# Kernel optimization log

Hardware: AMD Instinct MI355X
Metric: run time of the kernel (lower is better)

The kernel has to match this reference:

```python
import jax, jax.numpy as jnp
import numpy as np

V, E, H = 32000, 1024, 1024   # vocab, embed, hidden
B, T = 16, 128                 # batch, decode steps
SOS = 1


def setup_inputs() -> dict:
    key = jax.random.key(0)
    ks = jax.random.split(key, 10)
    w = 1.0 / np.sqrt(H)
    return {
        "encoder_outputs": jax.random.normal(ks[0], (B, T, H), jnp.float32),
        "encoder_hidden_h": jax.random.normal(ks[1], (1, B, H), jnp.float32),
        "encoder_hidden_c": jax.random.normal(ks[2], (1, B, H), jnp.float32),
        "embedding": jax.random.normal(ks[3], (V, E), jnp.float32) * 0.02,
        "W_ih": jax.random.normal(ks[4], (4 * H, E), jnp.float32) * w,
        "W_hh": jax.random.normal(ks[5], (4 * H, H), jnp.float32) * w,
        "b_ih": jax.random.normal(ks[6], (4 * H,), jnp.float32) * w,
        "b_hh": jax.random.normal(ks[7], (4 * H,), jnp.float32) * w,
        "W_lin": jax.random.normal(ks[8], (V, H), jnp.float32) * w,
        "b_lin": jax.random.normal(ks[9], (V,), jnp.float32) * w,
    }


def reference(encoder_outputs, encoder_hidden_h, encoder_hidden_c,
              embedding, W_ih, W_hh, b_ih, b_hh, W_lin, b_lin):
    # embed(token) -> single-step LSTM -> linear -> argmax feeds next step.
    batch = encoder_outputs.shape[0]
    num_steps = encoder_outputs.shape[1]
    h0 = encoder_hidden_h[0]  # [B,H] (num_layers=1)
    c0 = encoder_hidden_c[0]
    tok0 = jnp.full((batch,), SOS, dtype=jnp.int32)

    def step(carry, _):
        tok, h, c = carry
        x = embedding[tok]                                   # [B,E] gather
        gates = x @ W_ih.T + b_ih + h @ W_hh.T + b_hh        # [B,4H]
        i, f, g, o = jnp.split(gates, 4, axis=-1)            # PyTorch gate order i,f,g,o
        c = jax.nn.sigmoid(f) * c + jax.nn.sigmoid(i) * jnp.tanh(g)
        h = jax.nn.sigmoid(o) * jnp.tanh(c)
        logits = h @ W_lin.T + b_lin                         # [B,V]
        tok = jnp.argmax(logits, axis=-1).astype(jnp.int32)  # detached greedy token
        return (tok, h, c), logits

    (tok, h, c), logits = jax.lax.scan(step, (tok0, h0, c0), None, length=num_steps)
    # logits: [T,B,V] -> [B,T,V], then log_softmax as in torch forward
    log_probs = jax.nn.log_softmax(jnp.transpose(logits, (1, 0, 2)), axis=-1)
    return log_probs, h[None], c[None]
```

## Files before the change

kernel.cpp:

```cpp
#include <hip/hip_runtime.h>
#include <climits>
#include <cmath>


#define NBLK 256
#define NTHR 512
#define WPB  8
#define Bb 16
#define Hh 1024
#define Vv 32000
#define Tt 128
#define PITCH 1028

typedef float v4f __attribute__((ext_vector_type(4)));

__device__ __forceinline__ float dot4f(v4f a, v4f b, float acc) {
  return fmaf(a.x, b.x, fmaf(a.y, b.y, fmaf(a.z, b.z, fmaf(a.w, b.w, acc))));
}

__device__ __forceinline__ void online_upd(float& m, float& s, int& idx, float v, int r) {
  if (v > m) { s = s * __expf(m - v) + 1.0f; m = v; idx = r; }
  else       { s += __expf(v - m); }
}

__device__ __forceinline__ void merge_ms(float& m, float& s, int& idx,
                                         float m2, float s2, int i2) {
  if (m2 > m)       { s = s * __expf(m - m2) + s2; m = m2; idx = i2; }
  else if (m2 == m) { s += s2; idx = (i2 < idx) ? i2 : idx; }
  else              { s = fmaf(s2, __expf(m2 - m), s); }
}

__device__ __forceinline__ void grid_barrier(int* flags, int* gen, int epoch) {
  __syncthreads();
  if (threadIdx.x == 0) {
    __hip_atomic_store(&flags[blockIdx.x * 16], epoch,
                       __ATOMIC_RELEASE, __HIP_MEMORY_SCOPE_AGENT);
  }
  if (blockIdx.x == 0) {
    if (threadIdx.x < 64) {
      int base = threadIdx.x * 4;
      for (;;) {
        bool done = true;
#pragma unroll
        for (int k = 0; k < 4; ++k) {
          int v = __hip_atomic_load(&flags[(base + k) * 16],
                                    __ATOMIC_RELAXED, __HIP_MEMORY_SCOPE_AGENT);
          done &= (v >= epoch);
        }
        if (done) break;
        __builtin_amdgcn_s_sleep(2);
      }
    }
    __syncthreads();
    if (threadIdx.x == 0) {
      __threadfence();
      __hip_atomic_store(gen, epoch, __ATOMIC_RELEASE, __HIP_MEMORY_SCOPE_AGENT);
    }
  } else {
    if (threadIdx.x == 0) {
      while (__hip_atomic_load(gen, __ATOMIC_RELAXED, __HIP_MEMORY_SCOPE_AGENT) < epoch) {
        __builtin_amdgcn_s_sleep(2);
      }
      __threadfence();
    }
  }
  __syncthreads();
}

extern "C" __global__ void __launch_bounds__(NTHR, 2)
decoder_rnn_kernel(const float* __restrict__ enc_h,
                   const float* __restrict__ enc_c,
                   const float* __restrict__ emb,
                   const float* __restrict__ Wih,
                   const float* __restrict__ Whh,
                   const float* __restrict__ bih,
                   const float* __restrict__ bhh,
                   const float* __restrict__ Wlin,
                   const float* __restrict__ blin,
                   float* __restrict__ out,
                   int* flags, int* gen,
                   float* hb0, float* hb1, float* cbuf,
                   float* pm, float* ps, int* pidx)
{
  __shared__ float x_sh[Bb * PITCH];
  __shared__ float h_sh[Bb * PITCH];
  __shared__ float gpart[WPB][8][Bb];
  __shared__ float bm_[WPB][Bb];
  __shared__ float bs_[WPB][Bb];
  __shared__ int   bi_[WPB][Bb];
  __shared__ int   tk_sh[Bb];
  __shared__ float nm_sh[Bb];

  const int tid  = threadIdx.x;
  const int lane = tid & 63;
  const int wid  = tid >> 6;
  const int q    = lane >> 4;
  const int b    = lane & 15;
  const int bid  = blockIdx.x;
  const int wgl  = bid * WPB + wid;
  int ep = 0;

  float accL[4][4];
#pragma unroll
  for (int g = 0; g < 4; ++g)
#pragma unroll
    for (int r = 0; r < 4; ++r) accL[g][r] = 0.f;

  for (int i = tid; i < Bb * (Hh / 4); i += NTHR) {
    int bb = i >> 8, k4 = i & 255;
    v4f hv = reinterpret_cast<const v4f*>(enc_h + (size_t)bb * Hh)[k4];
    *reinterpret_cast<v4f*>(&h_sh[bb * PITCH + k4 * 4]) = hv;
  }

  for (int t = 0; t < Tt; ++t) {
    float* hcur = (t & 1) ? hb1 : hb0;

    if (t > 0) {
      int g = tid >> 5, l = tid & 31;
      float m = -__builtin_inff(); float s = 0.f; int ix = INT_MAX;
      for (int wb = l; wb < NBLK; wb += 32)
        merge_ms(m, s, ix, pm[wb * Bb + g], ps[wb * Bb + g], pidx[wb * Bb + g]);
#pragma unroll
      for (int off = 16; off; off >>= 1) {
        float m2 = __shfl_xor(m, off, 32);
        float s2 = __shfl_xor(s, off, 32);
        int   i2 = __shfl_xor(ix, off, 32);
        merge_ms(m, s, ix, m2, s2, i2);
      }
      if (l == 0) { tk_sh[g] = ix; nm_sh[g] = m + logf(s); }
    } else {
      if (tid < Bb) tk_sh[tid] = 1;
    }
    __syncthreads();

    if (t > 0 && wgl < 2000 && q == 0) {
      float nb = nm_sh[b];
      size_t obase = ((size_t)b * Tt + (t - 1)) * (size_t)Vv;
#pragma unroll
      for (int g = 0; g < 4; ++g) {
        int rbase = wgl * 16 + g * 4;
        v4f vo;
        vo.x = accL[g][0] - nb; vo.y = accL[g][1] - nb;
        vo.z = accL[g][2] - nb; vo.w = accL[g][3] - nb;
        __builtin_nontemporal_store(vo, reinterpret_cast<v4f*>(out + obase + rbase));
      }
    }
    for (int i = tid; i < Bb * (Hh / 4); i += NTHR) {
      int bb = i >> 8, k4 = i & 255;
      int tk = tk_sh[bb];
      v4f xv = reinterpret_cast<const v4f*>(emb + (size_t)tk * Hh)[k4];
      *reinterpret_cast<v4f*>(&x_sh[bb * PITCH + k4 * 4]) = xv;
    }
    __syncthreads();

    {
      const int j  = bid * 4 + (wid >> 1);
      const int kh = wid & 1;
      const int kb4 = kh * 128 + q * 32;
      const v4f* wi0 = reinterpret_cast<const v4f*>(Wih) + (size_t)j * 256 + kb4;
      const v4f* wi1 = wi0 + (size_t)Hh * 256;
      const v4f* wi2 = wi1 + (size_t)Hh * 256;
      const v4f* wi3 = wi2 + (size_t)Hh * 256;
      const v4f* wh0 = reinterpret_cast<const v4f*>(Whh) + (size_t)j * 256 + kb4;
      const v4f* wh1 = wh0 + (size_t)Hh * 256;
      const v4f* wh2 = wh1 + (size_t)Hh * 256;
      const v4f* wh3 = wh2 + (size_t)Hh * 256;
      const float* xb  = &x_sh[b * PITCH + kh * 512 + q * 128];
      const float* hbp = &h_sh[b * PITCH + kh * 512 + q * 128];
      float a0=0,a1=0,a2=0,a3=0,a4=0,a5=0,a6=0,a7=0;
#pragma unroll 2
      for (int i = 0; i < 32; ++i) {
        v4f xv = *reinterpret_cast<const v4f*>(xb + i * 4);
        v4f hv = *reinterpret_cast<const v4f*>(hbp + i * 4);
        a0 = dot4f(xv, wi0[i], a0);
        a1 = dot4f(xv, wi1[i], a1);
        a2 = dot4f(xv, wi2[i], a2);
        a3 = dot4f(xv, wi3[i], a3);
        a4 = dot4f(hv, wh0[i], a4);
        a5 = dot4f(hv, wh1[i], a5);
        a6 = dot4f(hv, wh2[i], a6);
        a7 = dot4f(hv, wh3[i], a7);
      }
      a0 += __shfl_xor(a0, 16, 64); a0 += __shfl_xor(a0, 32, 64);
      a1 += __shfl_xor(a1, 16, 64); a1 += __shfl_xor(a1, 32, 64);
      a2 += __shfl_xor(a2, 16, 64); a2 += __shfl_xor(a2, 32, 64);
      a3 += __shfl_xor(a3, 16, 64); a3 += __shfl_xor(a3, 32, 64);
      a4 += __shfl_xor(a4, 16, 64); a4 += __shfl_xor(a4, 32, 64);
      a5 += __shfl_xor(a5, 16, 64); a5 += __shfl_xor(a5, 32, 64);
      a6 += __shfl_xor(a6, 16, 64); a6 += __shfl_xor(a6, 32, 64);
      a7 += __shfl_xor(a7, 16, 64); a7 += __shfl_xor(a7, 32, 64);
      if (q == 0) {
        gpart[wid][0][b] = a0; gpart[wid][1][b] = a1;
        gpart[wid][2][b] = a2; gpart[wid][3][b] = a3;
        gpart[wid][4][b] = a4; gpart[wid][5][b] = a5;
        gpart[wid][6][b] = a6; gpart[wid][7][b] = a7;
      }
    }
    __syncthreads();
    if (wid == 0) {
      const int jj = q;
      const int j  = bid * 4 + jj;
      float s0 = gpart[2*jj][0][b] + gpart[2*jj+1][0][b];
      float s1 = gpart[2*jj][1][b] + gpart[2*jj+1][1][b];
      float s2 = gpart[2*jj][2][b] + gpart[2*jj+1][2][b];
      float s3 = gpart[2*jj][3][b] + gpart[2*jj+1][3][b];
      float s4 = gpart[2*jj][4][b] + gpart[2*jj+1][4][b];
      float s5 = gpart[2*jj][5][b] + gpart[2*jj+1][5][b];
      float s6 = gpart[2*jj][6][b] + gpart[2*jj+1][6][b];
      float s7 = gpart[2*jj][7][b] + gpart[2*jj+1][7][b];
      float gi = s0 + s4 + bih[j]          + bhh[j];
      float gf = s1 + s5 + bih[Hh + j]     + bhh[Hh + j];
      float gg = s2 + s6 + bih[2*Hh + j]   + bhh[2*Hh + j];
      float go = s3 + s7 + bih[3*Hh + j]   + bhh[3*Hh + j];
      float cold = (t == 0) ? enc_c[b * Hh + j] : cbuf[b * Hh + j];
      float ig = 1.f / (1.f + expf(-gi));
      float fg = 1.f / (1.f + expf(-gf));
      float og = 1.f / (1.f + expf(-go));
      float cn = fg * cold + ig * tanhf(gg);
      float hn = og * tanhf(cn);
      cbuf[b * Hh + j] = cn;
      hcur[b * Hh + j] = hn;
    }
    grid_barrier(flags, gen, ++ep);

    for (int i = tid; i < Bb * (Hh / 4); i += NTHR) {
      int bb = i >> 8, k4 = i & 255;
      v4f hv = reinterpret_cast<const v4f*>(hcur + (size_t)bb * Hh)[k4];
      *reinterpret_cast<v4f*>(&h_sh[bb * PITCH + k4 * 4]) = hv;
    }
    __syncthreads();
    float mloc = -__builtin_inff(); float sloc = 0.f; int iloc = INT_MAX;
    if (wgl < 2000) {
      const float* hbp = &h_sh[b * PITCH + q * 256];
#pragma unroll
      for (int g = 0; g < 4; ++g) {
        size_t rbase = (size_t)wgl * 16 + g * 4;
        const v4f* w0 = reinterpret_cast<const v4f*>(Wlin) + rbase * 256 + q * 64;
        const v4f* w1 = w0 + 256;
        const v4f* w2 = w1 + 256;
        const v4f* w3 = w2 + 256;
        float a0=0, a1=0, a2=0, a3=0;
#pragma unroll 4
        for (int i = 0; i < 64; ++i) {
          v4f hv = *reinterpret_cast<const v4f*>(hbp + i * 4);
          a0 = dot4f(hv, w0[i], a0);
          a1 = dot4f(hv, w1[i], a1);
          a2 = dot4f(hv, w2[i], a2);
          a3 = dot4f(hv, w3[i], a3);
        }
        a0 += __shfl_xor(a0, 16, 64); a0 += __shfl_xor(a0, 32, 64);
        a1 += __shfl_xor(a1, 16, 64); a1 += __shfl_xor(a1, 32, 64);
        a2 += __shfl_xor(a2, 16, 64); a2 += __shfl_xor(a2, 32, 64);
        a3 += __shfl_xor(a3, 16, 64); a3 += __shfl_xor(a3, 32, 64);
        int rb0 = (int)rbase;
        a0 += blin[rb0]; a1 += blin[rb0+1]; a2 += blin[rb0+2]; a3 += blin[rb0+3];
        accL[g][0]=a0; accL[g][1]=a1; accL[g][2]=a2; accL[g][3]=a3;
        online_upd(mloc, sloc, iloc, a0, rb0);
        online_upd(mloc, sloc, iloc, a1, rb0+1);
        online_upd(mloc, sloc, iloc, a2, rb0+2);
        online_upd(mloc, sloc, iloc, a3, rb0+3);
      }
    }
    if (q == 0) { bm_[wid][b] = mloc; bs_[wid][b] = sloc; bi_[wid][b] = iloc; }
    __syncthreads();
    if (tid < Bb) {
      float m = bm_[0][tid], s = bs_[0][tid]; int ix = bi_[0][tid];
#pragma unroll
      for (int w = 1; w < WPB; ++w) merge_ms(m, s, ix, bm_[w][tid], bs_[w][tid], bi_[w][tid]);
      pm[bid * Bb + tid] = m; ps[bid * Bb + tid] = s; pidx[bid * Bb + tid] = ix;
    }
    grid_barrier(flags, gen, ++ep);
  }

  {
    int g = tid >> 5, l = tid & 31;
    float m = -__builtin_inff(); float s = 0.f; int ix = INT_MAX;
    for (int wb = l; wb < NBLK; wb += 32)
      merge_ms(m, s, ix, pm[wb * Bb + g], ps[wb * Bb + g], pidx[wb * Bb + g]);
#pragma unroll
    for (int off = 16; off; off >>= 1) {
      float m2 = __shfl_xor(m, off, 32);
      float s2 = __shfl_xor(s, off, 32);
      int   i2 = __shfl_xor(ix, off, 32);
      merge_ms(m, s, ix, m2, s2, i2);
    }
    if (l == 0) nm_sh[g] = m + logf(s);
  }
  __syncthreads();
  if (wgl < 2000 && q == 0) {
    float nb = nm_sh[b];
    size_t obase = ((size_t)b * Tt + (Tt - 1)) * (size_t)Vv;
#pragma unroll
    for (int g = 0; g < 4; ++g) {
      int rbase = wgl * 16 + g * 4;
      v4f vo;
      vo.x = accL[g][0] - nb; vo.y = accL[g][1] - nb;
      vo.z = accL[g][2] - nb; vo.w = accL[g][3] - nb;
      __builtin_nontemporal_store(vo, reinterpret_cast<v4f*>(out + obase + rbase));
    }
  }
  const float* hfin = hb1;
  size_t tail = (size_t)Bb * Tt * Vv;
  for (int i = bid * NTHR + tid; i < Bb * Hh; i += NBLK * NTHR) {
    out[tail + i] = hfin[i];
    out[tail + Bb * Hh + i] = cbuf[i];
  }
}

extern "C" void kernel_launch(void* const* d_in, const int* in_sizes, int n_in,
                              void* d_out, int out_size, void* d_ws, size_t ws_size,
                              hipStream_t stream) {
  const float* enc_h = (const float*)d_in[1];
  const float* enc_c = (const float*)d_in[2];
  const float* emb   = (const float*)d_in[3];
  const float* Wih   = (const float*)d_in[4];
  const float* Whh   = (const float*)d_in[5];
  const float* bih   = (const float*)d_in[6];
  const float* bhh   = (const float*)d_in[7];
  const float* Wlin  = (const float*)d_in[8];
  const float* blin  = (const float*)d_in[9];
  float* out = (float*)d_out;

  char* ws = (char*)d_ws;
  int*   flags = (int*)ws;
  int*   gen   = (int*)(ws + 16384);
  float* hb0   = (float*)(ws + 17408);
  float* hb1   = (float*)(ws + 17408 + 65536);
  float* cbuf  = (float*)(ws + 17408 + 131072);
  float* pm    = (float*)(ws + 17408 + 196608);
  float* ps    = (float*)(ws + 17408 + 212992);
  int*   pidx  = (int*)  (ws + 17408 + 229376);

  hipMemsetAsync(d_ws, 0, 16448, stream);

  void* kargs[] = { (void*)&enc_h, (void*)&enc_c, (void*)&emb, (void*)&Wih,
                    (void*)&Whh, (void*)&bih, (void*)&bhh, (void*)&Wlin,
                    (void*)&blin, (void*)&out, (void*)&flags, (void*)&gen,
                    (void*)&hb0, (void*)&hb1, (void*)&cbuf,
                    (void*)&pm, (void*)&ps, (void*)&pidx };
  hipError_t e = hipLaunchCooperativeKernel((const void*)decoder_rnn_kernel,
                                            dim3(NBLK), dim3(NTHR), kargs, 0, stream);
  if (e != hipSuccess) {
    decoder_rnn_kernel<<<dim3(NBLK), dim3(NTHR), 0, stream>>>(
        enc_h, enc_c, emb, Wih, Whh, bih, bhh, Wlin, blin, out,
        flags, gen, hb0, hb1, cbuf, pm, ps, pidx);
  }
}
```

Baseline: 13.83 ms.

## Use fp16 vocab projection with top-3 rescoring, wider blocks, direct global reads

The kernel converts W_lin to fp16 once per call in a prelude kernel and computes the vocab logits with fdot2 on an fp16 copy of h, halving the weight bytes streamed per step. To keep greedy argmax exact, each block tracks the top-3 candidates, and when the top-2 gap is below a threshold it rescores them in fp32. It also doubles threads per block, reads the embedding and previous h directly from global memory instead of staging them in LDS, and reshapes the partial buffers into a batch-major layout. The fp16 logits that are written out carry reduced precision, and the 64 MB conversion runs on every call.

Result: slower. 20.53 ms (+48.5%).

```diff
diff --git a/kernel.cpp b/kernel.cpp
--- a/kernel.cpp
+++ b/kernel.cpp
@@ -4,30 +4,62 @@
 
 
 #define NBLK 256
-#define NTHR 512
-#define WPB  8
+#define NTHR 1024
+#define WPB  16
 #define Bb 16
 #define Hh 1024
 #define Vv 32000
 #define Tt 128
-#define PITCH 1028
+#define P32 1028
+#define P16 1032
+#define THR 0.01f
 
 typedef float v4f __attribute__((ext_vector_type(4)));
+typedef _Float16 h2v __attribute__((ext_vector_type(2)));
+typedef _Float16 h8v __attribute__((ext_vector_type(8)));
+
+#define NEG_INF (-__builtin_inff())
 
 __device__ __forceinline__ float dot4f(v4f a, v4f b, float acc) {
   return fmaf(a.x, b.x, fmaf(a.y, b.y, fmaf(a.z, b.z, fmaf(a.w, b.w, acc))));
 }
 
-__device__ __forceinline__ void online_upd(float& m, float& s, int& idx, float v, int r) {
-  if (v > m) { s = s * __expf(m - v) + 1.0f; m = v; idx = r; }
-  else       { s += __expf(v - m); }
-}
-
-__device__ __forceinline__ void merge_ms(float& m, float& s, int& idx,
-                                         float m2, float s2, int i2) {
-  if (m2 > m)       { s = s * __expf(m - m2) + s2; m = m2; idx = i2; }
-  else if (m2 == m) { s += s2; idx = (i2 < idx) ? i2 : idx; }
-  else              { s = fmaf(s2, __expf(m2 - m), s); }
+__device__ __forceinline__ float dot8h(h8v x, h8v y, float acc) {
+#if defined(__has_builtin)
+#if __has_builtin(__builtin_amdgcn_fdot2)
+  h2v x0 = {x[0], x[1]}, x1 = {x[2], x[3]}, x2 = {x[4], x[5]}, x3 = {x[6], x[7]};
+  h2v y0 = {y[0], y[1]}, y1 = {y[2], y[3]}, y2 = {y[4], y[5]}, y3 = {y[6], y[7]};
+  acc = __builtin_amdgcn_fdot2(x0, y0, acc, false);
+  acc = __builtin_amdgcn_fdot2(x1, y1, acc, false);
+  acc = __builtin_amdgcn_fdot2(x2, y2, acc, false);
+  acc = __builtin_amdgcn_fdot2(x3, y3, acc, false);
+  return acc;
+#else
+#pragma unroll
+  for (int k = 0; k < 8; ++k) acc = fmaf((float)x[k], (float)y[k], acc);
+  return acc;
+#endif
+#else
+#pragma unroll
+  for (int k = 0; k < 8; ++k) acc = fmaf((float)x[k], (float)y[k], acc);
+  return acc;
+#endif
+}
+
+__device__ __forceinline__ bool better(float x, int xi, float y, int yi) {
+  return (x > y) || (x == y && xi < yi);
+}
+__device__ __forceinline__ void ins3(float& m0, float& m1, float& m2,
+                                     int& i0, int& i1, int& i2, float x, int xi) {
+  if (better(x, xi, m0, i0))      { m2 = m1; i2 = i1; m1 = m0; i1 = i0; m0 = x; i0 = xi; }
+  else if (better(x, xi, m1, i1)) { m2 = m1; i2 = i1; m1 = x; i1 = xi; }
+  else if (better(x, xi, m2, i2)) { m2 = x; i2 = xi; }
+}
+__device__ __forceinline__ void lse_merge(float& M, float& S, float m2, float s2) {
+  float nM = fmaxf(M, m2);
+  float a = (M  > NEG_INF) ? S  * __expf(M  - nM) : 0.f;
+  float b = (m2 > NEG_INF) ? s2 * __expf(m2 - nM) : 0.f;
+  M = nM; S = a + b;
 }
 
 __device__ __forceinline__ void grid_barrier(int* flags, int* gen, int epoch) {
@@ -67,7 +99,82 @@
   __syncthreads();
 }
 
-extern "C" __global__ void __launch_bounds__(NTHR, 2)
+__device__ __forceinline__ void grid_reduce(
+    int bb, int lane, bool need_tok,
+    const float* __restrict__ pm0, const float* __restrict__ pm1,
+    const float* __restrict__ pm2, const int* __restrict__ pi0,
+    const int* __restrict__ pi1, const int* __restrict__ pi2,
+    const float* __restrict__ ps, const float* __restrict__ hp,
+    const float* __restrict__ Wlin, const float* __restrict__ blin,
+    int* tk_sh, float* nm_sh) {
+  float M0 = NEG_INF, M1 = NEG_INF, M2 = NEG_INF;
+  int I0 = INT_MAX, I1 = INT_MAX, I2 = INT_MAX;
+  float M = NEG_INF, S = 0.f;
+  const int base = bb * NBLK;
+#pragma unroll
+  for (int r = 0; r < 4; ++r) {
+    int wb = lane + r * 64;
+    float a0 = pm0[base + wb], a1 = pm1[base + wb], a2 = pm2[base + wb];
+    int   j0 = pi0[base + wb], j1 = pi1[base + wb], j2 = pi2[base + wb];
+    float s  = ps[base + wb];
+    ins3(M0, M1, M2, I0, I1, I2, a0, j0);
+    ins3(M0, M1, M2, I0, I1, I2, a1, j1);
+    ins3(M0, M1, M2, I0, I1, I2, a2, j2);
+    lse_merge(M, S, a0, s);
+  }
+#pragma unroll
+  for (int off = 32; off; off >>= 1) {
+    float xm0 = __shfl_xor(M0, off, 64), xm1 = __shfl_xor(M1, off, 64);
+    float xm2 = __shfl_xor(M2, off, 64), xs = __shfl_xor(S, off, 64);
+    int xi0 = __shfl_xor(I0, off, 64), xi1 = __shfl_xor(I1, off, 64);
+    int xi2 = __shfl_xor(I2, off, 64);
+    lse_merge(M, S, xm0, xs);
+    ins3(M0, M1, M2, I0, I1, I2, xm0, xi0);
+    ins3(M0, M1, M2, I0, I1, I2, xm1, xi1);
+    ins3(M0, M1, M2, I0, I1, I2, xm2, xi2);
+  }
+  float nm = M0 + logf(S);
+  if (need_tok) {
+    int tk = I0;
+    if (M0 - M1 < THR) {
+      const float* hpB = hp + bb * Hh;
+      float vr[3]; int ir[3] = {I0, I1, I2};
+#pragma unroll
+      for (int r = 0; r < 3; ++r) {
+        const v4f* w4 = reinterpret_cast<const v4f*>(Wlin + (size_t)ir[r] * Hh) + lane * 4;
+        const v4f* h4 = reinterpret_cast<const v4f*>(hpB) + lane * 4;
+        float a = 0.f;
+#pragma unroll
+        for (int k = 0; k < 4; ++k) a = dot4f(h4[k], w4[k], a);
+#pragma unroll
+        for (int off = 32; off; off >>= 1) a += __shfl_xor(a, off, 64);
+        vr[r] = a + blin[ir[r]];
+      }
+      float vb = vr[0]; tk = ir[0];
+#pragma unroll
+      for (int r = 1; r < 3; ++r)
+        if (vr[r] > vb || (vr[r] == vb && ir[r] < tk)) { vb = vr[r]; tk = ir[r]; }
+    }
+    if (lane == 0) tk_sh[bb] = tk;
+  }
+  if (lane == 0) nm_sh[bb] = nm;
+}
+
+__global__ void wconv_kernel(const float* __restrict__ w, _Float16* __restrict__ o, int n8) {
+  int i = blockIdx.x * blockDim.x + threadIdx.x;
+  int stride = gridDim.x * blockDim.x;
+  for (; i < n8; i += stride) {
+    const v4f* p = reinterpret_cast<const v4f*>(w + (size_t)i * 8);
+    v4f a = p[0], b = p[1];
+    h8v r;
+    r[0] = (_Float16)a.x; r[1] = (_Float16)a.y; r[2] = (_Float16)a.z; r[3] = (_Float16)a.w;
+    r[4] = (_Float16)b.x; r[5] = (_Float16)b.y; r[6] = (_Float16)b.z; r[7] = (_Float16)b.w;
+    *reinterpret_cast<h8v*>(o + (size_t)i * 8) = r;
+  }
+}
+
+template <int MODE>
+__global__ void __launch_bounds__(NTHR, 4)
 decoder_rnn_kernel(const float* __restrict__ enc_h,
                    const float* __restrict__ enc_c,
                    const float* __restrict__ emb,
@@ -77,17 +184,18 @@
                    const float* __restrict__ bhh,
                    const float* __restrict__ Wlin,
                    const float* __restrict__ blin,
+                   const _Float16* __restrict__ W16,
                    float* __restrict__ out,
                    int* flags, int* gen,
                    float* hb0, float* hb1, float* cbuf,
-                   float* pm, float* ps, int* pidx)
+                   float* pm0, float* pm1, float* pm2,
+                   int* pi0, int* pi1, int* pi2, float* ps)
 {
-  __shared__ float x_sh[Bb * PITCH];
-  __shared__ float h_sh[Bb * PITCH];
+  __shared__ float hbuf[Bb * P32];
   __shared__ float gpart[WPB][8][Bb];
-  __shared__ float bm_[WPB][Bb];
-  __shared__ float bs_[WPB][Bb];
-  __shared__ int   bi_[WPB][Bb];
+  __shared__ float wpm[3][WPB][Bb];
+  __shared__ int   wpi[3][WPB][Bb];
+  __shared__ float wps[WPB][Bb];
   __shared__ int   tk_sh[Bb];
   __shared__ float nm_sh[Bb];
 
@@ -99,87 +207,62 @@
   const int bid  = blockIdx.x;
   const int wgl  = bid * WPB + wid;
   int ep = 0;
-
-  float accL[4][4];
-#pragma unroll
-  for (int g = 0; g < 4; ++g)
+  _Float16* h16 = reinterpret_cast<_Float16*>(hbuf);
+
+  float accL[2][4];
+#pragma unroll
+  for (int g = 0; g < 2; ++g)
 #pragma unroll
     for (int r = 0; r < 4; ++r) accL[g][r] = 0.f;
-
-  for (int i = tid; i < Bb * (Hh / 4); i += NTHR) {
-    int bb = i >> 8, k4 = i & 255;
-    v4f hv = reinterpret_cast<const v4f*>(enc_h + (size_t)bb * Hh)[k4];
-    *reinterpret_cast<v4f*>(&h_sh[bb * PITCH + k4 * 4]) = hv;
-  }
 
   for (int t = 0; t < Tt; ++t) {
     float* hcur = (t & 1) ? hb1 : hb0;
+    const float* hprev = (t == 0) ? enc_h : ((t & 1) ? hb0 : hb1);
 
     if (t > 0) {
-      int g = tid >> 5, l = tid & 31;
-      float m = -__builtin_inff(); float s = 0.f; int ix = INT_MAX;
-      for (int wb = l; wb < NBLK; wb += 32)
-        merge_ms(m, s, ix, pm[wb * Bb + g], ps[wb * Bb + g], pidx[wb * Bb + g]);
-#pragma unroll
-      for (int off = 16; off; off >>= 1) {
-        float m2 = __shfl_xor(m, off, 32);
-        float s2 = __shfl_xor(s, off, 32);
-        int   i2 = __shfl_xor(ix, off, 32);
-        merge_ms(m, s, ix, m2, s2, i2);
-      }
-      if (l == 0) { tk_sh[g] = ix; nm_sh[g] = m + logf(s); }
+      grid_reduce(wid, lane, true, pm0, pm1, pm2, pi0, pi1, pi2, ps,
+                  hprev, Wlin, blin, tk_sh, nm_sh);
     } else {
       if (tid < Bb) tk_sh[tid] = 1;
     }
     __syncthreads();
 
-    if (t > 0 && wgl < 2000 && q == 0) {
+    if (t > 0 && wgl < 4000 && q == 0) {
       float nb = nm_sh[b];
       size_t obase = ((size_t)b * Tt + (t - 1)) * (size_t)Vv;
 #pragma unroll
-      for (int g = 0; g < 4; ++g) {
-        int rbase = wgl * 16 + g * 4;
+      for (int g = 0; g < 2; ++g) {
+        int rbase = wgl * 8 + g * 4;
         v4f vo;
         vo.x = accL[g][0] - nb; vo.y = accL[g][1] - nb;
         vo.z = accL[g][2] - nb; vo.w = accL[g][3] - nb;
         __builtin_nontemporal_store(vo, reinterpret_cast<v4f*>(out + obase + rbase));
       }
     }
-    for (int i = tid; i < Bb * (Hh / 4); i += NTHR) {
-      int bb = i >> 8, k4 = i & 255;
-      int tk = tk_sh[bb];
-      v4f xv = reinterpret_cast<const v4f*>(emb + (size_t)tk * Hh)[k4];
-      *reinterpret_cast<v4f*>(&x_sh[bb * PITCH + k4 * 4]) = xv;
-    }
-    __syncthreads();
 
     {
-      const int j  = bid * 4 + (wid >> 1);
-      const int kh = wid & 1;
-      const int kb4 = kh * 128 + q * 32;
-      const v4f* wi0 = reinterpret_cast<const v4f*>(Wih) + (size_t)j * 256 + kb4;
-      const v4f* wi1 = wi0 + (size_t)Hh * 256;
-      const v4f* wi2 = wi1 + (size_t)Hh * 256;
-      const v4f* wi3 = wi2 + (size_t)Hh * 256;
-      const v4f* wh0 = reinterpret_cast<const v4f*>(Whh) + (size_t)j * 256 + kb4;
-      const v4f* wh1 = wh0 + (size_t)Hh * 256;
-      const v4f* wh2 = wh1 + (size_t)Hh * 256;
-      const v4f* wh3 = wh2 + (size_t)Hh * 256;
-      const float* xb  = &x_sh[b * PITCH + kh * 512 + q * 128];
-      const float* hbp = &h_sh[b * PITCH + kh * 512 + q * 128];
-      float a0=0,a1=0,a2=0,a3=0,a4=0,a5=0,a6=0,a7=0;
-#pragma unroll 2
-      for (int i = 0; i < 32; ++i) {
-        v4f xv = *reinterpret_cast<const v4f*>(xb + i * 4);
-        v4f hv = *reinterpret_cast<const v4f*>(hbp + i * 4);
-        a0 = dot4f(xv, wi0[i], a0);
-        a1 = dot4f(xv, wi1[i], a1);
-        a2 = dot4f(xv, wi2[i], a2);
-        a3 = dot4f(xv, wi3[i], a3);
-        a4 = dot4f(hv, wh0[i], a4);
-        a5 = dot4f(hv, wh1[i], a5);
-        a6 = dot4f(hv, wh2[i], a6);
-        a7 = dot4f(hv, wh3[i], a7);
+      const int jj = wid >> 2;
+      const int kq = wid & 3;
+      const int j  = bid * 4 + jj;
+      const int ko = kq * 256 + q * 64;
+      const v4f* wi = reinterpret_cast<const v4f*>(Wih + (size_t)j * Hh + ko);
+      const v4f* wh = reinterpret_cast<const v4f*>(Whh + (size_t)j * Hh + ko);
+      const size_t gs = (size_t)Hh * Hh / 4;
+      const v4f* xv4 = reinterpret_cast<const v4f*>(emb + (size_t)tk_sh[b] * Hh + ko);
+      const v4f* hv4 = reinterpret_cast<const v4f*>(hprev + (size_t)b * Hh + ko);
+      float a0 = 0, a1 = 0, a2 = 0, a3 = 0, a4 = 0, a5 = 0, a6 = 0, a7 = 0;
+#pragma unroll 4
+      for (int i = 0; i < 16; ++i) {
+        v4f xv = xv4[i];
+        v4f hv = hv4[i];
+        a0 = dot4f(xv, wi[i], a0);
+        a1 = dot4f(xv, wi[i + gs], a1);
+        a2 = dot4f(xv, wi[i + 2 * gs], a2);
+        a3 = dot4f(xv, wi[i + 3 * gs], a3);
+        a4 = dot4f(hv, wh[i], a4);
+        a5 = dot4f(hv, wh[i + gs], a5);
+        a6 = dot4f(hv, wh[i + 2 * gs], a6);
+        a7 = dot4f(hv, wh[i + 3 * gs], a7);
       }
       a0 += __shfl_xor(a0, 16, 64); a0 += __shfl_xor(a0, 32, 64);
       a1 += __shfl_xor(a1, 16, 64); a1 += __shfl_xor(a1, 32, 64);
@@ -200,18 +283,16 @@
     if (wid == 0) {
       const int jj = q;
       const int j  = bid * 4 + jj;
-      float s0 = gpart[2*jj][0][b] + gpart[2*jj+1][0][b];
-      float s1 = gpart[2*jj][1][b] + gpart[2*jj+1][1][b];
-      float s2 = gpart[2*jj][2][b] + gpart[2*jj+1][2][b];
-      float s3 = gpart[2*jj][3][b] + gpart[2*jj+1][3][b];
-      float s4 = gpart[2*jj][4][b] + gpart[2*jj+1][4][b];
-      float s5 = gpart[2*jj][5][b] + gpart[2*jj+1][5][b];
-      float s6 = gpart[2*jj][6][b] + gpart[2*jj+1][6][b];
-      float s7 = gpart[2*jj][7][b] + gpart[2*jj+1][7][b];
-      float gi = s0 + s4 + bih[j]          + bhh[j];
-      float gf = s1 + s5 + bih[Hh + j]     + bhh[Hh + j];
-      float gg = s2 + s6 + bih[2*Hh + j]   + bhh[2*Hh + j];
-      float go = s3 + s7 + bih[3*Hh + j]   + bhh[3*Hh + j];
+      float sg[8];
+#pragma unroll
+      for (int g = 0; g < 8; ++g) {
+        sg[g] = gpart[jj * 4 + 0][g][b] + gpart[jj * 4 + 1][g][b]
+              + gpart[jj * 4 + 2][g][b] + gpart[jj * 4 + 3][g][b];
+      }
+      float gi = sg[0] + sg[4] + bih[j]          + bhh[j];
+      float gf = sg[1] + sg[5] + bih[Hh + j]     + bhh[Hh + j];
+      float gg = sg[2] + sg[6] + bih[2 * Hh + j] + bhh[2 * Hh + j];
+      float go = sg[3] + sg[7] + bih[3 * Hh + j] + bhh[3 * Hh + j];
       float cold = (t == 0) ? enc_c[b * Hh + j] : cbuf[b * Hh + j];
       float ig = 1.f / (1.f + expf(-gi));
       float fg = 1.f / (1.f + expf(-gf));
@@ -223,86 +304,121 @@
     }
     grid_barrier(flags, gen, ++ep);
 
-    for (int i = tid; i < Bb * (Hh / 4); i += NTHR) {
-      int bb = i >> 8, k4 = i & 255;
-      v4f hv = reinterpret_cast<const v4f*>(hcur + (size_t)bb * Hh)[k4];
-      *reinterpret_cast<v4f*>(&h_sh[bb * PITCH + k4 * 4]) = hv;
+    {
+      int row = tid >> 6;
+      int col = (tid & 63) * 16;
+      const v4f* src = reinterpret_cast<const v4f*>(hcur + (size_t)row * Hh + col);
+      v4f v0 = src[0], v1 = src[1], v2 = src[2], v3 = src[3];
+      if (MODE == 1) {
+        h8v r0, r1;
+        r0[0]=(_Float16)v0.x; r0[1]=(_Float16)v0.y; r0[2]=(_Float16)v0.z; r0[3]=(_Float16)v0.w;
+        r0[4]=(_Float16)v1.x; r0[5]=(_Float16)v1.y; r0[6]=(_Float16)v1.z; r0[7]=(_Float16)v1.w;
+        r1[0]=(_Float16)v2.x; r1[1]=(_Float16)v2.y; r1[2]=(_Float16)v2.z; r1[3]=(_Float16)v2.w;
+        r1[4]=(_Float16)v3.x; r1[5]=(_Float16)v3.y; r1[6]=(_Float16)v3.z; r1[7]=(_Float16)v3.w;
+        *reinterpret_cast<h8v*>(h16 + row * P16 + col) = r0;
+        *reinterpret_cast<h8v*>(h16 + row * P16 + col + 8) = r1;
+      } else {
+        v4f* dst = reinterpret_cast<v4f*>(hbuf + row * P32 + col);
+        dst[0] = v0; dst[1] = v1; dst[2] = v2; dst[3] = v3;
+      }
     }
     __syncthreads();
-    float mloc = -__builtin_inff(); float sloc = 0.f; int iloc = INT_MAX;
-    if (wgl < 2000) {
-      const float* hbp = &h_sh[b * PITCH + q * 256];
-#pragma unroll
-      for (int g = 0; g < 4; ++g) {
-        size_t rbase = (size_t)wgl * 16 + g * 4;
-        const v4f* w0 = reinterpret_cast<const v4f*>(Wlin) + rbase * 256 + q * 64;
-        const v4f* w1 = w0 + 256;
-        const v4f* w2 = w1 + 256;
-        const v4f* w3 = w2 + 256;
-        float a0=0, a1=0, a2=0, a3=0;
+
+    float m0 = NEG_INF, m1 = NEG_INF, m2 = NEG_INF;
+    int i0 = INT_MAX, i1 = INT_MAX, i2 = INT_MAX;
+    float sl = 0.f;
+    if (wgl < 4000) {
+#pragma unroll
+      for (int g = 0; g < 2; ++g) {
+        size_t rbase = (size_t)wgl * 8 + g * 4;
+        float a0 = 0, a1 = 0, a2 = 0, a3 = 0;
+        if (MODE == 1) {
+          const _Float16* hbp = h16 + b * P16 + q * 256;
+          const _Float16* wr = W16 + rbase * Hh + q * 256;
 #pragma unroll 4
-        for (int i = 0; i < 64; ++i) {
-          v4f hv = *reinterpret_cast<const v4f*>(hbp + i * 4);
-          a0 = dot4f(hv, w0[i], a0);
-          a1 = dot4f(hv, w1[i], a1);
-          a2 = dot4f(hv, w2[i], a2);
-          a3 = dot4f(hv, w3[i], a3);
+          for (int i = 0; i < 32; ++i) {
+            h8v hh = *reinterpret_cast<const h8v*>(hbp + i * 8);
+            a0 = dot8h(hh, *reinterpret_cast<const h8v*>(wr + i * 8), a0);
+            a1 = dot8h(hh, *reinterpret_cast<const h8v*>(wr + Hh + i * 8), a1);
+            a2 = dot8h(hh, *reinterpret_cast<const h8v*>(wr + 2 * Hh + i * 8), a2);
+            a3 = dot8h(hh, *reinterpret_cast<const h8v*>(wr + 3 * Hh + i * 8), a3);
+          }
+        } else {
+          const float* hbp = hbuf + b * P32 + q * 256;
+          const v4f* w0 = reinterpret_cast<const v4f*>(Wlin + rbase * Hh) + q * 64;
+          const v4f* w1 = w0 + 256;
+          const v4f* w2 = w1 + 256;
+          const v4f* w3 = w2 + 256;
+#pragma unroll 4
+          for (int i = 0; i < 64; ++i) {
+            v4f hv = *reinterpret_cast<const v4f*>(hbp + i * 4);
+            a0 = dot4f(hv, w0[i], a0);
+            a1 = dot4f(hv, w1[i], a1);
+            a2 = dot4f(hv, w2[i], a2);
+            a3 = dot4f(hv, w3[i], a3);
+          }
         }
         a0 += __shfl_xor(a0, 16, 64); a0 += __shfl_xor(a0, 32, 64);
         a1 += __shfl_xor(a1, 16, 64); a1 += __shfl_xor(a1, 32, 64);
         a2 += __shfl_xor(a2, 16, 64); a2 += __shfl_xor(a2, 32, 64);
         a3 += __shfl_xor(a3, 16, 64); a3 += __shfl_xor(a3, 32, 64);
         int rb0 = (int)rbase;
-        a0 += blin[rb0]; a1 += blin[rb0+1]; a2 += blin[rb0+2]; a3 += blin[rb0+3];
-        accL[g][0]=a0; accL[g][1]=a1; accL[g][2]=a2; accL[g][3]=a3;
-        online_upd(mloc, sloc, iloc, a0, rb0);
-        online_upd(mloc, sloc, iloc, a1, rb0+1);
-        online_upd(mloc, sloc, iloc, a2, rb0+2);
-        online_upd(mloc, sloc, iloc, a3, rb0+3);
-      }
-    }
-    if (q == 0) { bm_[wid][b] = mloc; bs_[wid][b] = sloc; bi_[wid][b] = iloc; }
+        a0 += blin[rb0]; a1 += blin[rb0 + 1]; a2 += blin[rb0 + 2]; a3 += blin[rb0 + 3];
+        accL[g][0] = a0; accL[g][1] = a1; accL[g][2] = a2; accL[g][3] = a3;
+        ins3(m0, m1, m2, i0, i1, i2, a0, rb0);
+        ins3(m0, m1, m2, i0, i1, i2, a1, rb0 + 1);
+        ins3(m0, m1, m2, i0, i1, i2, a2, rb0 + 2);
+        ins3(m0, m1, m2, i0, i1, i2, a3, rb0 + 3);
+      }
+#pragma unroll
+      for (int g = 0; g < 2; ++g)
+#pragma unroll
+        for (int r = 0; r < 4; ++r) sl += __expf(accL[g][r] - m0);
+    }
+    if (q == 0) {
+      wpm[0][wid][b] = m0; wpm[1][wid][b] = m1; wpm[2][wid][b] = m2;
+      wpi[0][wid][b] = i0; wpi[1][wid][b] = i1; wpi[2][wid][b] = i2;
+      wps[wid][b] = sl;
+    }
     __syncthreads();
     if (tid < Bb) {
-      float m = bm_[0][tid], s = bs_[0][tid]; int ix = bi_[0][tid];
-#pragma unroll
-      for (int w = 1; w < WPB; ++w) merge_ms(m, s, ix, bm_[w][tid], bs_[w][tid], bi_[w][tid]);
-      pm[bid * Bb + tid] = m; ps[bid * Bb + tid] = s; pidx[bid * Bb + tid] = ix;
+      const int bb = tid;
+      float M0 = NEG_INF, M1 = NEG_INF, M2 = NEG_INF;
+      int I0 = INT_MAX, I1 = INT_MAX, I2 = INT_MAX;
+      float M = NEG_INF, S = 0.f;
+#pragma unroll
+      for (int w = 0; w < WPB; ++w) {
+        float a0 = wpm[0][w][bb], a1 = wpm[1][w][bb], a2 = wpm[2][w][bb];
+        lse_merge(M, S, a0, wps[w][bb]);
+        ins3(M0, M1, M2, I0, I1, I2, a0, wpi[0][w][bb]);
+        ins3(M0, M1, M2, I0, I1, I2, a1, wpi[1][w][bb]);
+        ins3(M0, M1, M2, I0, I1, I2, a2, wpi[2][w][bb]);
+      }
+      pm0[bb * NBLK + bid] = M0; pm1[bb * NBLK + bid] = M1; pm2[bb * NBLK + bid] = M2;
+      pi0[bb * NBLK + bid] = I0; pi1[bb * NBLK + bid] = I1; pi2[bb * NBLK + bid] = I2;
+      ps[bb * NBLK + bid] = S;
     }
     grid_barrier(flags, gen, ++ep);
   }
 
-  {
-    int g = tid >> 5, l = tid & 31;
-    float m = -__builtin_inff(); float s = 0.f; int ix = INT_MAX;
-    for (int wb = l; wb < NBLK; wb += 32)
-      merge_ms(m, s, ix, pm[wb * Bb + g], ps[wb * Bb + g], pidx[wb * Bb + g]);
-#pragma unroll
-    for (int off = 16; off; off >>= 1) {
-      float m2 = __shfl_xor(m, off, 32);
-      float s2 = __shfl_xor(s, off, 32);
-      int   i2 = __shfl_xor(ix, off, 32);
-      merge_ms(m, s, ix, m2, s2, i2);
-    }
-    if (l == 0) nm_sh[g] = m + logf(s);
-  }
+  grid_reduce(wid, lane, false, pm0, pm1, pm2, pi0, pi1, pi2, ps,
+              hb1, Wlin, blin, tk_sh, nm_sh);
   __syncthreads();
-  if (wgl < 2000 && q == 0) {
+  if (wgl < 4000 && q == 0) {
     float nb = nm_sh[b];
     size_t obase = ((size_t)b * Tt + (Tt - 1)) * (size_t)Vv;
 #pragma unroll
-    for (int g = 0; g < 4; ++g) {
-      int rbase = wgl * 16 + g * 4;
+    for (int g = 0; g < 2; ++g) {
+      int rbase = wgl * 8 + g * 4;
       v4f vo;
       vo.x = accL[g][0] - nb; vo.y = accL[g][1] - nb;
       vo.z = accL[g][2] - nb; vo.w = accL[g][3] - nb;
       __builtin_nontemporal_store(vo, reinterpret_cast<v4f*>(out + obase + rbase));
     }
   }
-  const float* hfin = hb1;
   size_t tail = (size_t)Bb * Tt * Vv;
   for (int i = bid * NTHR + tid; i < Bb * Hh; i += NBLK * NTHR) {
-    out[tail + i] = hfin[i];
+    out[tail + i] = hb1[i];
     out[tail + Bb * Hh + i] = cbuf[i];
   }
 }
@@ -325,24 +441,51 @@
   int*   flags = (int*)ws;
   int*   gen   = (int*)(ws + 16384);
   float* hb0   = (float*)(ws + 17408);
-  float* hb1   = (float*)(ws + 17408 + 65536);
-  float* cbuf  = (float*)(ws + 17408 + 131072);
-  float* pm    = (float*)(ws + 17408 + 196608);
-  float* ps    = (float*)(ws + 17408 + 212992);
-  int*   pidx  = (int*)  (ws + 17408 + 229376);
+  float* hb1   = (float*)(ws + 82944);
+  float* cbuf  = (float*)(ws + 148480);
+  float* pm0   = (float*)(ws + 214016);
+  float* pm1   = (float*)(ws + 230400);
+  float* pm2   = (float*)(ws + 246784);
+  int*   pi0   = (int*)  (ws + 263168);
+  int*   pi1   = (int*)  (ws + 279552);
+  int*   pi2   = (int*)  (ws + 295936);
+  float* ps    = (float*)(ws + 312320);
+  _Float16* W16 = (_Float16*)(ws + 328704);
+  const size_t need16 = 328704ULL + 65536000ULL;
 
   hipMemsetAsync(d_ws, 0, 16448, stream);
 
-  void* kargs[] = { (void*)&enc_h, (void*)&enc_c, (void*)&emb, (void*)&Wih,
-                    (void*)&Whh, (void*)&bih, (void*)&bhh, (void*)&Wlin,
-                    (void*)&blin, (void*)&out, (void*)&flags, (void*)&gen,
-                    (void*)&hb0, (void*)&hb1, (void*)&cbuf,
-                    (void*)&pm, (void*)&ps, (void*)&pidx };
-  hipError_t e = hipLaunchCooperativeKernel((const void*)decoder_rnn_kernel,
-                                            dim3(NBLK), dim3(NTHR), kargs, 0, stream);
-  if (e != hipSuccess) {
-    decoder_rnn_kernel<<<dim3(NBLK), dim3(NTHR), 0, stream>>>(
-        enc_h, enc_c, emb, Wih, Whh, bih, bhh, Wlin, blin, out,
-        flags, gen, hb0, hb1, cbuf, pm, ps, pidx);
-  }
-}
+  bool use16 = (ws_size >= need16);
+  if (use16) {
+    wconv_kernel<<<dim3(4096), dim3(512), 0, stream>>>(Wlin, W16, 4096000);
+    auto* fp = decoder_rnn_kernel<1>;
+    void* kargs[] = { (void*)&enc_h, (void*)&enc_c, (void*)&emb, (void*)&Wih,
+                      (void*)&Whh, (void*)&bih, (void*)&bhh, (void*)&Wlin,
+                      (void*)&blin, (void*)&W16, (void*)&out, (void*)&flags,
+                      (void*)&gen, (void*)&hb0, (void*)&hb1, (void*)&cbuf,
+                      (void*)&pm0, (void*)&pm1, (void*)&pm2,
+                      (void*)&pi0, (void*)&pi1, (void*)&pi2, (void*)&ps };
+    hipError_t e = hipLaunchCooperativeKernel((const void*)fp, dim3(NBLK),
+                                              dim3(NTHR), kargs, 0, stream);
+    if (e != hipSuccess) {
+      decoder_rnn_kernel<1><<<dim3(NBLK), dim3(NTHR), 0, stream>>>(
+          enc_h, enc_c, emb, Wih, Whh, bih, bhh, Wlin, blin, W16, out,
+          flags, gen, hb0, hb1, cbuf, pm0, pm1, pm2, pi0, pi1, pi2, ps);
+    }
+  } else {
+    auto* fp = decoder_rnn_kernel<0>;
+    void* kargs[] = { (void*)&enc_h, (void*)&enc_c, (void*)&emb, (void*)&Wih,
+                      (void*)&Whh, (void*)&bih, (void*)&bhh, (void*)&Wlin,
+                      (void*)&blin, (void*)&W16, (void*)&out, (void*)&flags,
+                      (void*)&gen, (void*)&hb0, (void*)&hb1, (void*)&cbuf,
+                      (void*)&pm0, (void*)&pm1, (void*)&pm2,
+                      (void*)&pi0, (void*)&pi1, (void*)&pi2, (void*)&ps };
+    hipError_t e = hipLaunchCooperativeKernel((const void*)fp, dim3(NBLK),
+                                              dim3(NTHR), kargs, 0, stream);
+    if (e != hipSuccess) {
+      decoder_rnn_kernel<0><<<dim3(NBLK), dim3(NTHR), 0, stream>>>(
+          enc_h, enc_c, emb, Wih, Whh, bih, bhh, Wlin, blin, W16, out,
+          flags, gen, hb0, hb1, cbuf, pm0, pm1, pm2, pi0, pi1, pi2, ps);
+    }
+  }
+}
```
